# Kernel optimization log

Measured on AMD Instinct MI355X. Metric: run time of the kernel, lower is better.

## Reference

```python
import jax, jax.numpy as jnp
import numpy as np

QD = 512        # query_dim == key_dim
SD = 64         # spa_embed_dim
K = 4           # num_attn heads
EPS = 1e-6      # LayerNorm eps (space2vec LayerNorm)
SLOPE = 0.01    # nn.LeakyReLU default negative_slope


def setup_inputs() -> dict:
    key = jax.random.key(0)
    ks = jax.random.split(key, 6)
    B, N = 4096, 32
    D = 2 * QD + SD  # concat dim when have_query_embed=True
    xav = (6.0 / (D + K)) ** 0.5
    return {
        "key_embeds": jax.random.normal(ks[0], (B, N, QD), dtype=jnp.float32),
        "key_spa_embeds": jax.random.normal(ks[1], (B, N, SD), dtype=jnp.float32),
        "query_embed": jax.random.normal(ks[2], (B, QD), dtype=jnp.float32),
        "atten_vecs": jax.random.uniform(ks[3], (D, K), minval=-xav, maxval=xav, dtype=jnp.float32),
        "post_w": jax.random.normal(ks[4], (QD, QD), dtype=jnp.float32) * 0.02,
        "post_b": jnp.zeros((QD,), dtype=jnp.float32),
        "pre_ln_g": jnp.ones((QD,), dtype=jnp.float32),
        "pre_ln_b": jnp.zeros((QD,), dtype=jnp.float32),
        "post_ln_g": jnp.ones((QD,), dtype=jnp.float32),
        "post_ln_b": jnp.zeros((QD,), dtype=jnp.float32),
    }


def _layernorm(x, g, b):
    m = jnp.mean(x, axis=-1, keepdims=True)
    v = jnp.mean((x - m) ** 2, axis=-1, keepdims=True)
    return g * (x - m) / jnp.sqrt(v + EPS) + b


def reference(key_embeds, key_spa_embeds, query_embed, atten_vecs,
              post_w, post_b, pre_ln_g, pre_ln_b, post_ln_g, post_ln_b):
    B, N, _ = key_embeds.shape
    # expand query over context points and concat: [B, N, 2*QD+SD]
    q_exp = jnp.broadcast_to(query_embed[:, None, :], (B, N, QD))
    concat = jnp.concatenate([q_exp, key_embeds, key_spa_embeds], axis=2)
    # attention logits per head: [B, N, K]
    attn = jnp.einsum('bnd,dk->bnk', concat, atten_vecs)
    attn = jax.nn.leaky_relu(attn, SLOPE)
    attn = jax.nn.softmax(attn, axis=1)  # softmax over context points
    # weighted sum per head, then average over heads: [B, QD]
    combined = jnp.einsum('bnk,bnd->bkd', attn, key_embeds).sum(axis=1) * (1.0 / K)
    combined = jax.nn.sigmoid(combined)
    # pre layernorm with residual from query
    combined = _layernorm(combined + query_embed, pre_ln_g, pre_ln_b)
    # post linear (dropout in eval mode = identity) + residual + post LN
    lin = combined @ post_w.T + post_b
    out = _layernorm(lin + combined, post_ln_g, post_ln_b)
    return out
```

## Files before the change

kernel.cpp:

```cpp
#include <hip/hip_runtime.h>
#include <hip/hip_bf16.h>

#define QD 512
#define SD 64
#define NCTX 32
#define ROWA 1088
#define ROWB 1152

constexpr float EPS_LN = 1e-6f;
constexpr float SLOPE = 0.01f;

typedef __attribute__((ext_vector_type(8))) __bf16 bf16x8;
typedef __attribute__((ext_vector_type(4))) float f32x4;

__device__ __forceinline__ float red64(float v) {
#pragma unroll
    for (int m = 32; m; m >>= 1) v += __shfl_xor(v, m, 64);
    return v;
}

__device__ __forceinline__ float b2f(unsigned short u) {
    unsigned int x = ((unsigned int)u) << 16;
    return __builtin_bit_cast(float, x);
}
__device__ __forceinline__ unsigned short f2bu(float f) {
    __hip_bfloat16 h = __float2bfloat16(f);
    return __builtin_bit_cast(unsigned short, h);
}

__device__ __forceinline__ bf16x8 pack8(float4 a, float4 b) {
    bf16x8 r;
    r[0] = (__bf16)a.x; r[1] = (__bf16)a.y; r[2] = (__bf16)a.z; r[3] = (__bf16)a.w;
    r[4] = (__bf16)b.x; r[5] = (__bf16)b.y; r[6] = (__bf16)b.z; r[7] = (__bf16)b.w;
    return r;
}

__global__ __launch_bounds__(256, 4) void attn_fuse(
    const float* __restrict__ key, const float* __restrict__ spa,
    const float* __restrict__ query, const float* __restrict__ av,
    const float* __restrict__ lng, const float* __restrict__ lnb,
    float* __restrict__ yout,
    const float* __restrict__ postw, unsigned short* __restrict__ wb16)
{
    __shared__ __align__(16) unsigned char s_A[NCTX * ROWA];
    __shared__ __align__(16) unsigned char s_B[4 * ROWB];
    __shared__ float s_logit[NCTX][4];
    __shared__ float s_w[NCTX];
    __shared__ float s_red[8];
    __shared__ float s_ql[4];

    const int b = blockIdx.x;
    const int t = threadIdx.x;
    const int wave = t >> 6;
    const int lane = t & 63;

    const float* kb = key + (size_t)b * (NCTX * QD);
    const float* qb = query + (size_t)b * QD;
    const float* sb = spa + (size_t)b * (NCTX * SD);
    const float4* av4 = reinterpret_cast<const float4*>(av);

    if (t < 16) {
        const float4 wv = reinterpret_cast<const float4*>(postw)[b * 16 + t];
        ushort4 h;
        h.x = f2bu(wv.x); h.y = f2bu(wv.y); h.z = f2bu(wv.z); h.w = f2bu(wv.w);
        reinterpret_cast<ushort4*>(wb16)[b * 16 + t] = h;
    }

#pragma unroll
    for (int pass = 0; pass < 2; ++pass) {
        float4 kr[8];
#pragma unroll
        for (int i = 0; i < 4; ++i) {
            const float* krow = kb + (8 * wave + 4 * pass + i) * QD;
            kr[2 * i]     = reinterpret_cast<const float4*>(krow)[2 * lane];
            kr[2 * i + 1] = reinterpret_cast<const float4*>(krow)[2 * lane + 1];
        }
#pragma unroll
        for (int i = 0; i < 4; ++i) {
            const int n = 8 * wave + 4 * pass + i;
            *reinterpret_cast<bf16x8*>(&s_A[n * ROWA + 16 * lane]) =
                pack8(kr[2 * i], kr[2 * i + 1]);
        }
    }
    float4 sp0a, sp0b, sp1a, sp1b;
    if (wave < 2) {
        const int arow = 16 * wave + (lane & 15);
        const int qq8 = (lane >> 4) * 8;
        const float* s0p = sb + arow * SD + qq8;
        const float* s1p = sb + arow * SD + 32 + qq8;
        sp0a = reinterpret_cast<const float4*>(s0p)[0];
        sp0b = reinterpret_cast<const float4*>(s0p)[1];
        sp1a = reinterpret_cast<const float4*>(s1p)[0];
        sp1b = reinterpret_cast<const float4*>(s1p)[1];
    }
    float avreg[9];
#pragma unroll
    for (int r = 0; r < 9; ++r)
        avreg[r] = av[(size_t)(512 + lane * 9 + r) * 4 + wave];
#pragma unroll
    for (int r = 0; r < 9; ++r) {
        const int k = lane * 9 + r;
        *reinterpret_cast<__bf16*>(&s_B[wave * ROWB + ((2 * k) ^ (wave << 4))]) =
            (__bf16)avreg[r];
    }

    if (wave == 3) {
        const float4* q4 = reinterpret_cast<const float4*>(qb);
        float s0 = 0.f, s1 = 0.f, s2 = 0.f, s3 = 0.f;
#pragma unroll
        for (int h = 0; h < 2; ++h) {
            const float4 qv = q4[2 * lane + h];
            const float4 a0 = av4[8 * lane + 4 * h + 0];
            const float4 a1 = av4[8 * lane + 4 * h + 1];
            const float4 a2 = av4[8 * lane + 4 * h + 2];
            const float4 a3 = av4[8 * lane + 4 * h + 3];
            s0 += qv.x * a0.x + qv.y * a1.x + qv.z * a2.x + qv.w * a3.x;
            s1 += qv.x * a0.y + qv.y * a1.y + qv.z * a2.y + qv.w * a3.y;
            s2 += qv.x * a0.z + qv.y * a1.z + qv.z * a2.z + qv.w * a3.z;
            s3 += qv.x * a0.w + qv.y * a1.w + qv.z * a2.w + qv.w * a3.w;
        }
        s0 = red64(s0); s1 = red64(s1); s2 = red64(s2); s3 = red64(s3);
        if (lane == 0) { s_ql[0] = s0; s_ql[1] = s1; s_ql[2] = s2; s_ql[3] = s3; }
    }
    __syncthreads();

    if (wave < 2) {
        const int colB = lane & 15;
        const int kgrp = (lane >> 4) * 16;
        const int arow = 16 * wave + (lane & 15);
        f32x4 acc = {0.f, 0.f, 0.f, 0.f};
        bf16x8 bz;
#pragma unroll
        for (int e = 0; e < 8; ++e) bz[e] = (__bf16)0.0f;
#pragma unroll
        for (int ks = 0; ks < 16; ++ks) {
            const int koff = ks * 64 + kgrp;
            const bf16x8 af =
                *reinterpret_cast<const bf16x8*>(&s_A[arow * ROWA + koff]);
            bf16x8 bf = bz;
            if (colB < 4)
                bf = *reinterpret_cast<const bf16x8*>(
                    &s_B[colB * ROWB + (koff ^ (colB << 4))]);
            acc = __builtin_amdgcn_mfma_f32_16x16x32_bf16(af, bf, acc, 0, 0, 0);
        }
#pragma unroll
        for (int ks = 0; ks < 2; ++ks) {
            const int koff = 1024 + ks * 64 + kgrp;
            const bf16x8 af = (ks == 0) ? pack8(sp0a, sp0b) : pack8(sp1a, sp1b);
            bf16x8 bf = bz;
            if (colB < 4)
                bf = *reinterpret_cast<const bf16x8*>(
                    &s_B[colB * ROWB + (koff ^ (colB << 4))]);
            acc = __builtin_amdgcn_mfma_f32_16x16x32_bf16(af, bf, acc, 0, 0, 0);
        }
        if (colB < 4) {
            const float qlk = s_ql[colB];
#pragma unroll
            for (int r = 0; r < 4; ++r) {
                const int row = 16 * wave + (lane >> 4) * 4 + r;
                float v = acc[r] + qlk;
                v = v > 0.f ? v : SLOPE * v;
                s_logit[row][colB] = v;
            }
        }
    }
    __syncthreads();

    if (wave == 0) {
        const int n = lane & 31;
        float v0 = s_logit[n][0], v1 = s_logit[n][1],
              v2 = s_logit[n][2], v3 = s_logit[n][3];
        float m0 = v0, m1 = v1, m2 = v2, m3 = v3;
#pragma unroll
        for (int m = 16; m; m >>= 1) {
            m0 = fmaxf(m0, __shfl_xor(m0, m, 32));
            m1 = fmaxf(m1, __shfl_xor(m1, m, 32));
            m2 = fmaxf(m2, __shfl_xor(m2, m, 32));
            m3 = fmaxf(m3, __shfl_xor(m3, m, 32));
        }
        float e0 = __expf(v0 - m0), e1 = __expf(v1 - m1),
              e2 = __expf(v2 - m2), e3 = __expf(v3 - m3);
        float st0 = e0, st1 = e1, st2 = e2, st3 = e3;
#pragma unroll
        for (int m = 16; m; m >>= 1) {
            st0 += __shfl_xor(st0, m, 32);
            st1 += __shfl_xor(st1, m, 32);
            st2 += __shfl_xor(st2, m, 32);
            st3 += __shfl_xor(st3, m, 32);
        }
        const float w = 0.25f * (e0 / st0 + e1 / st1 + e2 / st2 + e3 / st3);
        if (lane < 32) s_w[n] = w;
    }
    __syncthreads();

    const int d0 = 2 * t;
    float acc0 = 0.f, acc1 = 0.f;
#pragma unroll
    for (int n = 0; n < NCTX; ++n) {
        const float wn = s_w[n];
        const unsigned int u =
            *reinterpret_cast<const unsigned int*>(&s_A[n * ROWA + 4 * t]);
        acc0 += wn * b2f((unsigned short)(u & 0xffffu));
        acc1 += wn * b2f((unsigned short)(u >> 16));
    }
    const float2 qv = *reinterpret_cast<const float2*>(&qb[d0]);
    const float x0 = 1.f / (1.f + __expf(-acc0)) + qv.x;
    const float x1 = 1.f / (1.f + __expf(-acc1)) + qv.y;

    float sum = red64(x0 + x1);
    float ssq = red64(x0 * x0 + x1 * x1);
    if (lane == 0) { s_red[wave] = sum; s_red[4 + wave] = ssq; }
    __syncthreads();
    sum = s_red[0] + s_red[1] + s_red[2] + s_red[3];
    ssq = s_red[4] + s_red[5] + s_red[6] + s_red[7];
    const float mean = sum * (1.f / QD);
    const float var = ssq * (1.f / QD) - mean * mean;
    const float inv = rsqrtf(var + EPS_LN);
    const float2 gg = *reinterpret_cast<const float2*>(&lng[d0]);
    const float2 bb = *reinterpret_cast<const float2*>(&lnb[d0]);
    float2 o;
    o.x = gg.x * (x0 - mean) * inv + bb.x;
    o.y = gg.y * (x1 - mean) * inv + bb.y;
    *reinterpret_cast<float2*>(&yout[(size_t)b * QD + d0]) = o;
}

__device__ __forceinline__ int swzB(int row, int off) {
    return row * 128 + (off ^ ((row & 7) << 4));
}

__global__ __launch_bounds__(256) void post_gemm(
    const float* __restrict__ Y, const unsigned short* __restrict__ Wb,
    const float* __restrict__ pbias, float* __restrict__ out)
{
    __shared__ __align__(16) unsigned char Ys[64 * 128];
    __shared__ __align__(16) unsigned char Ws[64 * 128];
    const int t = threadIdx.x;
    const int wave = t >> 6, lane = t & 63;
    const int bm = blockIdx.x * 64;
    const int bn = blockIdx.y * 64;

    const int lr = t >> 2;
    const int lq = (t & 3) * 16;

    f32x4 acc[4] = {{0.f,0.f,0.f,0.f},{0.f,0.f,0.f,0.f},
                    {0.f,0.f,0.f,0.f},{0.f,0.f,0.f,0.f}};

    for (int kc = 0; kc < QD; kc += 64) {
        float4 ya[4];
        const float* yrow = Y + (size_t)(bm + lr) * QD + kc + lq;
        const unsigned short* wrow = Wb + (size_t)(bn + lr) * QD + kc + lq;
#pragma unroll
        for (int j = 0; j < 4; ++j)
            ya[j] = reinterpret_cast<const float4*>(yrow)[j];
        const uint4 wa = reinterpret_cast<const uint4*>(wrow)[0];
        const uint4 wb = reinterpret_cast<const uint4*>(wrow)[1];
        __syncthreads();
        const int base = lq * 2;
        *reinterpret_cast<bf16x8*>(&Ys[swzB(lr, base)])      = pack8(ya[0], ya[1]);
        *reinterpret_cast<bf16x8*>(&Ys[swzB(lr, base + 16)]) = pack8(ya[2], ya[3]);
        *reinterpret_cast<uint4*>(&Ws[swzB(lr, base)])       = wa;
        *reinterpret_cast<uint4*>(&Ws[swzB(lr, base + 16)])  = wb;
        __syncthreads();
#pragma unroll
        for (int ks = 0; ks < 2; ++ks) {
            const int ko = ks * 64 + (lane >> 4) * 16;
            const bf16x8 af = *reinterpret_cast<const bf16x8*>(
                &Ys[swzB(16 * wave + (lane & 15), ko)]);
#pragma unroll
            for (int c = 0; c < 4; ++c) {
                const bf16x8 bf = *reinterpret_cast<const bf16x8*>(
                    &Ws[swzB(16 * c + (lane & 15), ko)]);
                acc[c] = __builtin_amdgcn_mfma_f32_16x16x32_bf16(af, bf, acc[c],
                                                                 0, 0, 0);
            }
        }
    }
    const int m0 = bm + 16 * wave + (lane >> 4) * 4;
#pragma unroll
    for (int c = 0; c < 4; ++c) {
        const int n = bn + 16 * c + (lane & 15);
        const float pb = pbias[n];
#pragma unroll
        for (int r = 0; r < 4; ++r) {
            const size_t idx = (size_t)(m0 + r) * QD + n;
            out[idx] = acc[c][r] + pb + Y[idx];
        }
    }
}

__global__ __launch_bounds__(256) void post_ln_kernel(
    float* __restrict__ out,
    const float* __restrict__ lng, const float* __restrict__ lnb)
{
    __shared__ float s_red[8];
    const int r = blockIdx.x;
    const int t = threadIdx.x;
    const int wave = t >> 6, lane = t & 63;
    const int d0 = 2 * t;
    const float2 lv = *reinterpret_cast<const float2*>(&out[(size_t)r * QD + d0]);
    const float x0 = lv.x;
    const float x1 = lv.y;
    float sum = red64(x0 + x1);
    float ssq = red64(x0 * x0 + x1 * x1);
    if (lane == 0) { s_red[wave] = sum; s_red[4 + wave] = ssq; }
    __syncthreads();
    sum = s_red[0] + s_red[1] + s_red[2] + s_red[3];
    ssq = s_red[4] + s_red[5] + s_red[6] + s_red[7];
    const float mean = sum * (1.f / QD);
    const float var = ssq * (1.f / QD) - mean * mean;
    const float inv = rsqrtf(var + EPS_LN);
    const float2 gg = *reinterpret_cast<const float2*>(&lng[d0]);
    const float2 bb = *reinterpret_cast<const float2*>(&lnb[d0]);
    float2 o;
    o.x = gg.x * (x0 - mean) * inv + bb.x;
    o.y = gg.y * (x1 - mean) * inv + bb.y;
    *reinterpret_cast<float2*>(&out[(size_t)r * QD + d0]) = o;
}

extern "C" void kernel_launch(void* const* d_in, const int* in_sizes, int n_in,
                              void* d_out, int out_size, void* d_ws, size_t ws_size,
                              hipStream_t stream) {
    const float* key    = (const float*)d_in[0];
    const float* spa    = (const float*)d_in[1];
    const float* query  = (const float*)d_in[2];
    const float* av     = (const float*)d_in[3];
    const float* postw  = (const float*)d_in[4];
    const float* postb  = (const float*)d_in[5];
    const float* pre_g  = (const float*)d_in[6];
    const float* pre_b  = (const float*)d_in[7];
    const float* post_g = (const float*)d_in[8];
    const float* post_b = (const float*)d_in[9];
    float* out = (float*)d_out;
    float* yws = (float*)d_ws;
    unsigned short* wb16 =
        (unsigned short*)((char*)d_ws + (8u << 20));

    const int B = in_sizes[2] / QD;

    attn_fuse<<<B, 256, 0, stream>>>(key, spa, query, av, pre_g, pre_b, yws,
                                     postw, wb16);
    dim3 gridB(B / 64, QD / 64);
    post_gemm<<<gridB, 256, 0, stream>>>(yws, wb16, postb, out);
    post_ln_kernel<<<B, 256, 0, stream>>>(out, post_g, post_b);
}
```

Baseline: 81.88 us.

## Process two batch rows per block with software-pipelined key loads

The attention kernel now handles two batch rows per block, using a double-buffered shared-memory key tile. Global loads for the second row's keys and spatial embeddings are issued while the first row's MFMA, softmax and weighted-sum phases run. The goal is to hide global-memory latency inside each block. In exchange, shared memory per block roughly doubles, the occupancy hint drops from 4 to 2 blocks, and the grid is halved, which could reduce latency hiding across blocks.

```diff
diff --git a/kernel.cpp b/kernel.cpp
--- a/kernel.cpp
+++ b/kernel.cpp
@@ -6,6 +6,7 @@
 #define NCTX 32
 #define ROWA 1088
 #define ROWB 1152
+#define ABUF (NCTX * ROWA)
 
 constexpr float EPS_LN = 1e-6f;
 constexpr float SLOPE = 0.01f;
@@ -35,171 +36,147 @@
     return r;
 }
 
-__global__ __launch_bounds__(256, 4) void attn_fuse(
-    const float* __restrict__ key, const float* __restrict__ spa,
-    const float* __restrict__ query, const float* __restrict__ av,
-    const float* __restrict__ lng, const float* __restrict__ lnb,
-    float* __restrict__ yout,
-    const float* __restrict__ postw, unsigned short* __restrict__ wb16)
-{
-    __shared__ __align__(16) unsigned char s_A[NCTX * ROWA];
-    __shared__ __align__(16) unsigned char s_B[4 * ROWB];
-    __shared__ float s_logit[NCTX][4];
-    __shared__ float s_w[NCTX];
-    __shared__ float s_red[8];
-    __shared__ float s_ql[4];
-
-    const int b = blockIdx.x;
-    const int t = threadIdx.x;
-    const int wave = t >> 6;
-    const int lane = t & 63;
-
-    const float* kb = key + (size_t)b * (NCTX * QD);
-    const float* qb = query + (size_t)b * QD;
-    const float* sb = spa + (size_t)b * (NCTX * SD);
-    const float4* av4 = reinterpret_cast<const float4*>(av);
-
-    if (t < 16) {
-        const float4 wv = reinterpret_cast<const float4*>(postw)[b * 16 + t];
-        ushort4 h;
-        h.x = f2bu(wv.x); h.y = f2bu(wv.y); h.z = f2bu(wv.z); h.w = f2bu(wv.w);
-        reinterpret_cast<ushort4*>(wb16)[b * 16 + t] = h;
-    }
-
-#pragma unroll
-    for (int pass = 0; pass < 2; ++pass) {
-        float4 kr[8];
-#pragma unroll
-        for (int i = 0; i < 4; ++i) {
-            const float* krow = kb + (8 * wave + 4 * pass + i) * QD;
-            kr[2 * i]     = reinterpret_cast<const float4*>(krow)[2 * lane];
-            kr[2 * i + 1] = reinterpret_cast<const float4*>(krow)[2 * lane + 1];
-        }
-#pragma unroll
-        for (int i = 0; i < 4; ++i) {
-            const int n = 8 * wave + 4 * pass + i;
-            *reinterpret_cast<bf16x8*>(&s_A[n * ROWA + 16 * lane]) =
-                pack8(kr[2 * i], kr[2 * i + 1]);
-        }
-    }
-    float4 sp0a, sp0b, sp1a, sp1b;
+struct SpFrag { float4 a0, b0, a1, b1; };
+
+__device__ __forceinline__ void load_pass(const float* kb, int wave, int lane,
+                                          int pass, float4 kr[8]) {
+#pragma unroll
+    for (int i = 0; i < 4; ++i) {
+        const float* krow = kb + (8 * wave + 4 * pass + i) * QD;
+        kr[2 * i]     = reinterpret_cast<const float4*>(krow)[2 * lane];
+        kr[2 * i + 1] = reinterpret_cast<const float4*>(krow)[2 * lane + 1];
+    }
+}
+__device__ __forceinline__ void write_pass(unsigned char* sA, int wave, int lane,
+                                           int pass, const float4 kr[8]) {
+#pragma unroll
+    for (int i = 0; i < 4; ++i) {
+        const int n = 8 * wave + 4 * pass + i;
+        *reinterpret_cast<bf16x8*>(&sA[n * ROWA + 16 * lane]) =
+            pack8(kr[2 * i], kr[2 * i + 1]);
+    }
+}
+__device__ __forceinline__ SpFrag load_sp(const float* sb, int wave, int lane) {
+    SpFrag s;
+    s.a0 = s.b0 = s.a1 = s.b1 = make_float4(0.f, 0.f, 0.f, 0.f);
     if (wave < 2) {
         const int arow = 16 * wave + (lane & 15);
         const int qq8 = (lane >> 4) * 8;
         const float* s0p = sb + arow * SD + qq8;
         const float* s1p = sb + arow * SD + 32 + qq8;
-        sp0a = reinterpret_cast<const float4*>(s0p)[0];
-        sp0b = reinterpret_cast<const float4*>(s0p)[1];
-        sp1a = reinterpret_cast<const float4*>(s1p)[0];
-        sp1b = reinterpret_cast<const float4*>(s1p)[1];
-    }
-    float avreg[9];
-#pragma unroll
-    for (int r = 0; r < 9; ++r)
-        avreg[r] = av[(size_t)(512 + lane * 9 + r) * 4 + wave];
-#pragma unroll
-    for (int r = 0; r < 9; ++r) {
-        const int k = lane * 9 + r;
-        *reinterpret_cast<__bf16*>(&s_B[wave * ROWB + ((2 * k) ^ (wave << 4))]) =
-            (__bf16)avreg[r];
-    }
-
-    if (wave == 3) {
-        const float4* q4 = reinterpret_cast<const float4*>(qb);
-        float s0 = 0.f, s1 = 0.f, s2 = 0.f, s3 = 0.f;
-#pragma unroll
-        for (int h = 0; h < 2; ++h) {
-            const float4 qv = q4[2 * lane + h];
-            const float4 a0 = av4[8 * lane + 4 * h + 0];
-            const float4 a1 = av4[8 * lane + 4 * h + 1];
-            const float4 a2 = av4[8 * lane + 4 * h + 2];
-            const float4 a3 = av4[8 * lane + 4 * h + 3];
-            s0 += qv.x * a0.x + qv.y * a1.x + qv.z * a2.x + qv.w * a3.x;
-            s1 += qv.x * a0.y + qv.y * a1.y + qv.z * a2.y + qv.w * a3.y;
-            s2 += qv.x * a0.z + qv.y * a1.z + qv.z * a2.z + qv.w * a3.z;
-            s3 += qv.x * a0.w + qv.y * a1.w + qv.z * a2.w + qv.w * a3.w;
+        s.a0 = reinterpret_cast<const float4*>(s0p)[0];
+        s.b0 = reinterpret_cast<const float4*>(s0p)[1];
+        s.a1 = reinterpret_cast<const float4*>(s1p)[0];
+        s.b1 = reinterpret_cast<const float4*>(s1p)[1];
+    }
+    return s;
+}
+__device__ __forceinline__ void ql_compute(const float* qb, const float4* av4,
+                                           float* dst, int lane) {
+    const float4* q4 = reinterpret_cast<const float4*>(qb);
+    float s0 = 0.f, s1 = 0.f, s2 = 0.f, s3 = 0.f;
+#pragma unroll
+    for (int h = 0; h < 2; ++h) {
+        const float4 qv = q4[2 * lane + h];
+        const float4 a0 = av4[8 * lane + 4 * h + 0];
+        const float4 a1 = av4[8 * lane + 4 * h + 1];
+        const float4 a2 = av4[8 * lane + 4 * h + 2];
+        const float4 a3 = av4[8 * lane + 4 * h + 3];
+        s0 += qv.x * a0.x + qv.y * a1.x + qv.z * a2.x + qv.w * a3.x;
+        s1 += qv.x * a0.y + qv.y * a1.y + qv.z * a2.y + qv.w * a3.y;
+        s2 += qv.x * a0.z + qv.y * a1.z + qv.z * a2.z + qv.w * a3.z;
+        s3 += qv.x * a0.w + qv.y * a1.w + qv.z * a2.w + qv.w * a3.w;
+    }
+    s0 = red64(s0); s1 = red64(s1); s2 = red64(s2); s3 = red64(s3);
+    if (lane == 0) { dst[0] = s0; dst[1] = s1; dst[2] = s2; dst[3] = s3; }
+}
+
+__device__ __forceinline__ void mfma_phase(
+    const unsigned char* sA, const unsigned char* sB, const SpFrag& sp,
+    const float* ql4, float (*s_logit)[4], int wave, int lane)
+{
+    if (wave >= 2) return;
+    const int colB = lane & 15;
+    const int kgrp = (lane >> 4) * 16;
+    const int arow = 16 * wave + (lane & 15);
+    f32x4 acc = {0.f, 0.f, 0.f, 0.f};
+    bf16x8 bz;
+#pragma unroll
+    for (int e = 0; e < 8; ++e) bz[e] = (__bf16)0.0f;
+#pragma unroll
+    for (int ks = 0; ks < 16; ++ks) {
+        const int koff = ks * 64 + kgrp;
+        const bf16x8 af =
+            *reinterpret_cast<const bf16x8*>(&sA[arow * ROWA + koff]);
+        bf16x8 bf = bz;
+        if (colB < 4)
+            bf = *reinterpret_cast<const bf16x8*>(
+                &sB[colB * ROWB + (koff ^ (colB << 4))]);
+        acc = __builtin_amdgcn_mfma_f32_16x16x32_bf16(af, bf, acc, 0, 0, 0);
+    }
+#pragma unroll
+    for (int ks = 0; ks < 2; ++ks) {
+        const int koff = 1024 + ks * 64 + kgrp;
+        const bf16x8 af = (ks == 0) ? pack8(sp.a0, sp.b0) : pack8(sp.a1, sp.b1);
+        bf16x8 bf = bz;
+        if (colB < 4)
+            bf = *reinterpret_cast<const bf16x8*>(
+                &sB[colB * ROWB + (koff ^ (colB << 4))]);
+        acc = __builtin_amdgcn_mfma_f32_16x16x32_bf16(af, bf, acc, 0, 0, 0);
+    }
+    if (colB < 4) {
+        const float qlk = ql4[colB];
+#pragma unroll
+        for (int r = 0; r < 4; ++r) {
+            const int row = 16 * wave + (lane >> 4) * 4 + r;
+            float v = acc[r] + qlk;
+            v = v > 0.f ? v : SLOPE * v;
+            s_logit[row][colB] = v;
         }
-        s0 = red64(s0); s1 = red64(s1); s2 = red64(s2); s3 = red64(s3);
-        if (lane == 0) { s_ql[0] = s0; s_ql[1] = s1; s_ql[2] = s2; s_ql[3] = s3; }
-    }
-    __syncthreads();
-
-    if (wave < 2) {
-        const int colB = lane & 15;
-        const int kgrp = (lane >> 4) * 16;
-        const int arow = 16 * wave + (lane & 15);
-        f32x4 acc = {0.f, 0.f, 0.f, 0.f};
-        bf16x8 bz;
-#pragma unroll
-        for (int e = 0; e < 8; ++e) bz[e] = (__bf16)0.0f;
-#pragma unroll
-        for (int ks = 0; ks < 16; ++ks) {
-            const int koff = ks * 64 + kgrp;
-            const bf16x8 af =
-                *reinterpret_cast<const bf16x8*>(&s_A[arow * ROWA + koff]);
-            bf16x8 bf = bz;
-            if (colB < 4)
-                bf = *reinterpret_cast<const bf16x8*>(
-                    &s_B[colB * ROWB + (koff ^ (colB << 4))]);
-            acc = __builtin_amdgcn_mfma_f32_16x16x32_bf16(af, bf, acc, 0, 0, 0);
-        }
-#pragma unroll
-        for (int ks = 0; ks < 2; ++ks) {
-            const int koff = 1024 + ks * 64 + kgrp;
-            const bf16x8 af = (ks == 0) ? pack8(sp0a, sp0b) : pack8(sp1a, sp1b);
-            bf16x8 bf = bz;
-            if (colB < 4)
-                bf = *reinterpret_cast<const bf16x8*>(
-                    &s_B[colB * ROWB + (koff ^ (colB << 4))]);
-            acc = __builtin_amdgcn_mfma_f32_16x16x32_bf16(af, bf, acc, 0, 0, 0);
-        }
-        if (colB < 4) {
-            const float qlk = s_ql[colB];
-#pragma unroll
-            for (int r = 0; r < 4; ++r) {
-                const int row = 16 * wave + (lane >> 4) * 4 + r;
-                float v = acc[r] + qlk;
-                v = v > 0.f ? v : SLOPE * v;
-                s_logit[row][colB] = v;
-            }
-        }
-    }
-    __syncthreads();
-
-    if (wave == 0) {
-        const int n = lane & 31;
-        float v0 = s_logit[n][0], v1 = s_logit[n][1],
-              v2 = s_logit[n][2], v3 = s_logit[n][3];
-        float m0 = v0, m1 = v1, m2 = v2, m3 = v3;
-#pragma unroll
-        for (int m = 16; m; m >>= 1) {
-            m0 = fmaxf(m0, __shfl_xor(m0, m, 32));
-            m1 = fmaxf(m1, __shfl_xor(m1, m, 32));
-            m2 = fmaxf(m2, __shfl_xor(m2, m, 32));
-            m3 = fmaxf(m3, __shfl_xor(m3, m, 32));
-        }
-        float e0 = __expf(v0 - m0), e1 = __expf(v1 - m1),
-              e2 = __expf(v2 - m2), e3 = __expf(v3 - m3);
-        float st0 = e0, st1 = e1, st2 = e2, st3 = e3;
-#pragma unroll
-        for (int m = 16; m; m >>= 1) {
-            st0 += __shfl_xor(st0, m, 32);
-            st1 += __shfl_xor(st1, m, 32);
-            st2 += __shfl_xor(st2, m, 32);
-            st3 += __shfl_xor(st3, m, 32);
-        }
-        const float w = 0.25f * (e0 / st0 + e1 / st1 + e2 / st2 + e3 / st3);
-        if (lane < 32) s_w[n] = w;
-    }
-    __syncthreads();
-
+    }
+}
+
+__device__ __forceinline__ void softmax_phase(
+    float (*s_logit)[4], float* s_w, int wave, int lane)
+{
+    if (wave != 0) return;
+    const int n = lane & 31;
+    float v0 = s_logit[n][0], v1 = s_logit[n][1],
+          v2 = s_logit[n][2], v3 = s_logit[n][3];
+    float m0 = v0, m1 = v1, m2 = v2, m3 = v3;
+#pragma unroll
+    for (int m = 16; m; m >>= 1) {
+        m0 = fmaxf(m0, __shfl_xor(m0, m, 32));
+        m1 = fmaxf(m1, __shfl_xor(m1, m, 32));
+        m2 = fmaxf(m2, __shfl_xor(m2, m, 32));
+        m3 = fmaxf(m3, __shfl_xor(m3, m, 32));
+    }
+    float e0 = __expf(v0 - m0), e1 = __expf(v1 - m1),
+          e2 = __expf(v2 - m2), e3 = __expf(v3 - m3);
+    float st0 = e0, st1 = e1, st2 = e2, st3 = e3;
+#pragma unroll
+    for (int m = 16; m; m >>= 1) {
+        st0 += __shfl_xor(st0, m, 32);
+        st1 += __shfl_xor(st1, m, 32);
+        st2 += __shfl_xor(st2, m, 32);
+        st3 += __shfl_xor(st3, m, 32);
+    }
+    const float w = 0.25f * (e0 / st0 + e1 / st1 + e2 / st2 + e3 / st3);
+    if (lane < 32) s_w[n] = w;
+}
+
+__device__ __forceinline__ void wsum_phase(
+    const unsigned char* sA, const float* s_w, const float* qb,
+    const float* lng, const float* lnb, float* yrow,
+    float* s_red, int wave, int lane, int t)
+{
     const int d0 = 2 * t;
     float acc0 = 0.f, acc1 = 0.f;
 #pragma unroll
     for (int n = 0; n < NCTX; ++n) {
         const float wn = s_w[n];
         const unsigned int u =
-            *reinterpret_cast<const unsigned int*>(&s_A[n * ROWA + 4 * t]);
+            *reinterpret_cast<const unsigned int*>(&sA[n * ROWA + 4 * t]);
         acc0 += wn * b2f((unsigned short)(u & 0xffffu));
         acc1 += wn * b2f((unsigned short)(u >> 16));
     }
@@ -221,7 +198,92 @@
     float2 o;
     o.x = gg.x * (x0 - mean) * inv + bb.x;
     o.y = gg.y * (x1 - mean) * inv + bb.y;
-    *reinterpret_cast<float2*>(&yout[(size_t)b * QD + d0]) = o;
+    *reinterpret_cast<float2*>(&yrow[d0]) = o;
+}
+
+__global__ __launch_bounds__(256, 2) void attn_fuse(
+    const float* __restrict__ key, const float* __restrict__ spa,
+    const float* __restrict__ query, const float* __restrict__ av,
+    const float* __restrict__ lng, const float* __restrict__ lnb,
+    float* __restrict__ yout,
+    const float* __restrict__ postw, unsigned short* __restrict__ wb16)
+{
+    __shared__ __align__(16) unsigned char s_A[2 * ABUF];
+    __shared__ __align__(16) unsigned char s_B[4 * ROWB];
+    __shared__ float s_logit[NCTX][4];
+    __shared__ float s_w[NCTX];
+    __shared__ float s_red[8];
+    __shared__ float s_ql[2][4];
+
+    const int g = blockIdx.x;
+    const int b0 = 2 * g, b1 = 2 * g + 1;
+    const int t = threadIdx.x;
+    const int wave = t >> 6;
+    const int lane = t & 63;
+
+    const float* kb0 = key + (size_t)b0 * (NCTX * QD);
+    const float* kb1 = key + (size_t)b1 * (NCTX * QD);
+    const float* qb0 = query + (size_t)b0 * QD;
+    const float* qb1 = query + (size_t)b1 * QD;
+    const float* sb0 = spa + (size_t)b0 * (NCTX * SD);
+    const float* sb1 = spa + (size_t)b1 * (NCTX * SD);
+    const float4* av4 = reinterpret_cast<const float4*>(av);
+    unsigned char* sA0 = s_A;
+    unsigned char* sA1 = s_A + ABUF;
+
+    if (t < 32) {
+        const int idx = g * 32 + t;
+        const float4 wv = reinterpret_cast<const float4*>(postw)[idx];
+        ushort4 h;
+        h.x = f2bu(wv.x); h.y = f2bu(wv.y); h.z = f2bu(wv.z); h.w = f2bu(wv.w);
+        reinterpret_cast<ushort4*>(wb16)[idx] = h;
+    }
+
+    {
+        float4 kr[8];
+        load_pass(kb0, wave, lane, 0, kr); write_pass(sA0, wave, lane, 0, kr);
+        load_pass(kb0, wave, lane, 1, kr); write_pass(sA0, wave, lane, 1, kr);
+    }
+    SpFrag spc = load_sp(sb0, wave, lane);
+    {
+        float avreg[9];
+#pragma unroll
+        for (int r = 0; r < 9; ++r)
+            avreg[r] = av[(size_t)(512 + lane * 9 + r) * 4 + wave];
+#pragma unroll
+        for (int r = 0; r < 9; ++r) {
+            const int k = lane * 9 + r;
+            *reinterpret_cast<__bf16*>(
+                &s_B[wave * ROWB + ((2 * k) ^ (wave << 4))]) = (__bf16)avreg[r];
+        }
+    }
+    if (wave == 3) ql_compute(qb0, av4, s_ql[0], lane);
+    __syncthreads();
+
+    float4 p0[8];
+    load_pass(kb1, wave, lane, 0, p0);
+    SpFrag spn = load_sp(sb1, wave, lane);
+    if (wave == 3) ql_compute(qb1, av4, s_ql[1], lane);
+    mfma_phase(sA0, s_B, spc, s_ql[0], s_logit, wave, lane);
+    __syncthreads();
+
+    write_pass(sA1, wave, lane, 0, p0);
+    float4 p1[8];
+    load_pass(kb1, wave, lane, 1, p1);
+    softmax_phase(s_logit, s_w, wave, lane);
+    __syncthreads();
+
+    wsum_phase(sA0, s_w, qb0, lng, lnb, yout + (size_t)b0 * QD,
+               s_red, wave, lane, t);
+    write_pass(sA1, wave, lane, 1, p1);
+    __syncthreads();
+
+    mfma_phase(sA1, s_B, spn, s_ql[1], s_logit, wave, lane);
+    __syncthreads();
+    softmax_phase(s_logit, s_w, wave, lane);
+    __syncthreads();
+    wsum_phase(sA1, s_w, qb1, lng, lnb, yout + (size_t)b1 * QD,
+               s_red, wave, lane, t);
 }
 
 __device__ __forceinline__ int swzB(int row, int off) {
@@ -337,8 +399,8 @@
 
     const int B = in_sizes[2] / QD;
 
-    attn_fuse<<<B, 256, 0, stream>>>(key, spa, query, av, pre_g, pre_b, yws,
-                                     postw, wb16);
+    attn_fuse<<<B / 2, 256, 0, stream>>>(key, spa, query, av, pre_g, pre_b,
+                                         yws, postw, wb16);
     dim3 gridB(B / 64, QD / 64);
     post_gemm<<<gridB, 256, 0, stream>>>(yws, wb16, postb, out);
     post_ln_kernel<<<B, 256, 0, stream>>>(out, post_g, post_b);
```

After: 88.08 us. 7.6% more time.
